# Kernel tuning notes

Measured on AMD Instinct MI355X. Metric: run time of the kernel, lower is better.

The kernel has to match this reference:

```python
import jax, jax.numpy as jnp
import numpy as np

N = 100000
D = 128
R = 4
E = 1600000
LN_EPS = 1e-3  # keras LayerNormalization default epsilon


def setup_inputs() -> dict:
    key = jax.random.key(0)
    ks = jax.random.split(key, 12)
    return {
        "node_embeddings": jax.random.normal(ks[0], (N, D), jnp.float32),
        "rel_embeddings": jax.random.normal(ks[1], (R, D), jnp.float32),
        "adj_rows": jax.random.randint(ks[2], (R, E), 0, N, jnp.int32),
        "adj_cols": jax.random.randint(ks[3], (R, E), 0, N, jnp.int32),
        "adj_vals": jax.random.uniform(ks[4], (R, E), jnp.float32),
        "W_fuse": jax.random.normal(ks[5], (2 * D, D), jnp.float32) * 0.05,
        "b_fuse": jnp.zeros((D,), jnp.float32),
        "W_rel": jax.random.normal(ks[6], (R, D, D), jnp.float32) * 0.05,
        "b_rel": jnp.zeros((R, D), jnp.float32),
        "rel_weights": jnp.ones((R,), jnp.float32),
        "W_gate": jax.random.normal(ks[7], (D, D), jnp.float32) * 0.05,
        "b_gate": jnp.zeros((D,), jnp.float32),
        "ln_gamma": jnp.ones((D,), jnp.float32),
        "ln_beta": jnp.zeros((D,), jnp.float32),
    }


def reference(node_embeddings, rel_embeddings, adj_rows, adj_cols, adj_vals,
              W_fuse, b_fuse, W_rel, b_rel, rel_weights, W_gate, b_gate,
              ln_gamma, ln_beta):
    n = node_embeddings.shape[0]
    rel_outs = []
    for r in range(R):  # small fixed relation count, structurally distinct kernels
        # sparse-dense matmul: messages[i] = sum_j A_r[i,j] * X[j]
        gathered = adj_vals[r][:, None] * node_embeddings[adj_cols[r]]  # [E, D]
        messages = jax.ops.segment_sum(gathered, adj_rows[r], num_segments=n)  # [N, D]
        rel_vec = jnp.broadcast_to(rel_embeddings[r], messages.shape)
        cat = jnp.concatenate([messages, rel_vec], axis=-1)  # [N, 2D]
        fused = jax.nn.relu(cat @ W_fuse + b_fuse)  # [N, D]
        rel_outs.append(fused @ W_rel[r] + b_rel[r])  # relation-specific kernel
    stacked = jnp.stack(rel_outs, axis=0)  # [R, N, D]
    w = jax.nn.softmax(rel_weights)
    combined = jnp.einsum('r,rnd->nd', w, stacked)
    gate = jax.nn.sigmoid(node_embeddings @ W_gate + b_gate)
    x = node_embeddings + gate * combined
    mu = jnp.mean(x, axis=-1, keepdims=True)
    var = jnp.mean((x - mu) ** 2, axis=-1, keepdims=True)
    out = (x - mu) * jax.lax.rsqrt(var + LN_EPS) * ln_gamma + ln_beta
    return out  # dropout is identity at inference (training=None)
```

## Files before the change

### kernel.cpp

```cpp
#include <hip/hip_runtime.h>
#include <math.h>

#define N_NODES 100000
#define DIM 128
#define NREL 4
#define NEDGE 1600000
#define LN_EPS 1e-3f

#define NBUCK 196
#define BCAP 10240
#define P1_VPT 16
#define P1_EDGES 4096

typedef __attribute__((ext_vector_type(8))) short bf16x8;
typedef __attribute__((ext_vector_type(4))) float f32x4;

__device__ __forceinline__ float bf2f(unsigned short b) {
    return __uint_as_float(((unsigned int)b) << 16);
}
__device__ __forceinline__ unsigned short f2bf(float f) {
    unsigned int u = __float_as_uint(f);
    u += 0x7FFFu + ((u >> 16) & 1u);
    return (unsigned short)(u >> 16);
}

__global__ __launch_bounds__(512) void prep_kernel(
    const float* __restrict__ rel_emb, const float* __restrict__ W_fuse,
    const float* __restrict__ b_fuse, const float* __restrict__ rel_weights,
    float* __restrict__ bfr, float* __restrict__ wsm)
{
    int t = threadIdx.x;
    int r = t >> 7;
    int d = t & 127;
    float acc = b_fuse[d];
    for (int k = 0; k < DIM; ++k)
        acc += rel_emb[r * DIM + k] * W_fuse[(DIM + k) * DIM + d];
    bfr[r * DIM + d] = acc;
    if (t < NREL) {
        float m = rel_weights[0];
        for (int i = 1; i < NREL; ++i) m = fmaxf(m, rel_weights[i]);
        float s = 0.f;
        for (int i = 0; i < NREL; ++i) s += expf(rel_weights[i] - m);
        wsm[t] = expf(rel_weights[t] - m) / s;
    }
}

__global__ __launch_bounds__(256) void pack_kernel(
    const float* __restrict__ Wf, const float* __restrict__ Wr,
    const float* __restrict__ Wg,
    unsigned short* __restrict__ PH, unsigned short* __restrict__ PL)
{
    int mat = blockIdx.y;
    int idx = blockIdx.x * 256 + threadIdx.x;
    int j = idx & 7;
    int lane = (idx >> 3) & 63;
    int ntile = (idx >> 9) & 7;
    int kblk = idx >> 12;
    int k = kblk * 32 + (lane >> 4) * 8 + j;
    int n = ntile * 16 + (lane & 15);
    const float* src = (mat == 0) ? Wf :
                       (mat == 5) ? Wg : (Wr + (size_t)(mat - 1) * DIM * DIM);
    float w = src[k * DIM + n];
    unsigned short hi = f2bf(w);
    float lo = w - bf2f(hi);
    PH[mat * 16384 + idx] = hi;
    PL[mat * 16384 + idx] = f2bf(lo);
}

__global__ __launch_bounds__(256) void xb_kernel(
    const float* __restrict__ X, unsigned short* __restrict__ Xb)
{
    int idx = blockIdx.x * 256 + threadIdx.x;
    float4 f = ((const float4*)X)[idx];
    ushort4 o;
    o.x = f2bf(f.x); o.y = f2bf(f.y); o.z = f2bf(f.z); o.w = f2bf(f.w);
    ((ushort4*)Xb)[idx] = o;
}

__global__ __launch_bounds__(256) void binA_kernel(
    const int* __restrict__ arows, const int* __restrict__ acols,
    const float* __restrict__ avals,
    int* __restrict__ bcnt,
    unsigned long long* __restrict__ edges2)
{
    __shared__ int hist[256];
    __shared__ int hoff[256];
    __shared__ int gbase[NBUCK];
    __shared__ unsigned long long stage[P1_EDGES];
    __shared__ unsigned short sbid[P1_EDGES];

    int t = threadIdx.x;
    int rl = blockIdx.y;
    int e0 = blockIdx.x * P1_EDGES;

    hist[t] = 0;
    __syncthreads();

    int b[P1_VPT], rank[P1_VPT], rloc[P1_VPT];
    unsigned int pay[P1_VPT];
#pragma unroll
    for (int i = 0; i < P1_VPT; ++i) {
        int e = e0 + i * 256 + t;
        b[i] = -1;
        if (e < NEDGE) {
            size_t off = (size_t)rl * NEDGE + e;
            int row = arows[off];
            unsigned int vb = __float_as_uint(avals[off]);
            vb += 0x7FFFu + ((vb >> 16) & 1u);
            pay[i] = ((unsigned int)acols[off] << 15) | ((vb >> 16) & 0x7FFFu);
            b[i] = row >> 9;
            rloc[i] = row & 511;
            rank[i] = atomicAdd(&hist[b[i]], 1);
        }
    }
    __syncthreads();

    int v = hist[t];
    int run = v;
    hoff[t] = run;
    __syncthreads();
    for (int o = 1; o < 256; o <<= 1) {
        int other = (t >= o) ? hoff[t - o] : 0;
        __syncthreads();
        run += other;
        hoff[t] = run;
        __syncthreads();
    }
    hoff[t] = run - v;
    if (t < NBUCK) {
        int g = (v > 0) ? atomicAdd(&bcnt[rl * NBUCK + t], v) : 0;
        gbase[t] = (rl * NBUCK + t) * BCAP + g;
    }
    __syncthreads();

#pragma unroll
    for (int i = 0; i < P1_VPT; ++i) {
        if (b[i] >= 0) {
            int slot = hoff[b[i]] + rank[i];
            stage[slot] = ((unsigned long long)rloc[i] << 32) | pay[i];
            sbid[slot] = (unsigned short)b[i];
        }
    }
    __syncthreads();

    int total = hoff[NBUCK - 1] + hist[NBUCK - 1];
    for (int idx = t; idx < total; idx += 256) {
        int bb = sbid[idx];
        int gaddr = gbase[bb] + (idx - hoff[bb]);
        if (gaddr - (rl * NBUCK + bb) * BCAP < BCAP)
            edges2[gaddr] = stage[idx];
    }
}

__global__ __launch_bounds__(1024) void bscan_kernel(
    const int* __restrict__ bcnt, int* __restrict__ bstart)
{
    __shared__ int s[1024];
    int t = threadIdx.x;
    int v = (t < NREL * NBUCK) ? min(bcnt[t], BCAP) : 0;
    int run = v;
    s[t] = run;
    __syncthreads();
    for (int o = 1; o < 1024; o <<= 1) {
        int other = (t >= o) ? s[t - o] : 0;
        __syncthreads();
        run += other;
        s[t] = run;
        __syncthreads();
    }
    if (t < NREL * NBUCK) bstart[t] = run - v;
}

__global__ __launch_bounds__(256) void binB_kernel(
    const unsigned long long* __restrict__ edges2,
    const int* __restrict__ bcnt, const int* __restrict__ bstart,
    int* __restrict__ rowstart, unsigned int* __restrict__ edges)
{
    __shared__ int rcnt[512];
    __shared__ int rpos[512];
    __shared__ int sc[256];

    int t = threadIdx.x;
    int b = blockIdx.x, rl = blockIdx.y;
    int gb = rl * NBUCK + b;
    int cnt = min(bcnt[gb], BCAP);
    const unsigned long long* src = edges2 + (size_t)gb * BCAP;
    int row0 = b << 9;
    int nrows = min(512, N_NODES - row0);

    rcnt[t] = 0; rcnt[t + 256] = 0;
    __syncthreads();
    for (int e = t; e < cnt; e += 256)
        atomicAdd(&rcnt[(int)(src[e] >> 32)], 1);
    __syncthreads();

    int v0 = rcnt[2 * t], v1 = rcnt[2 * t + 1];
    int tsum = v0 + v1;
    int run = tsum;
    sc[t] = run;
    __syncthreads();
    for (int o = 1; o < 256; o <<= 1) {
        int other = (t >= o) ? sc[t - o] : 0;
        __syncthreads();
        run += other;
        sc[t] = run;
        __syncthreads();
    }
    int base = bstart[gb];
    int excl = base + run - tsum;
    rpos[2 * t] = excl;
    rpos[2 * t + 1] = excl + v0;
    __syncthreads();

    for (int i = t; i < nrows; i += 256)
        rowstart[rl * N_NODES + row0 + i] = rpos[i];
    __syncthreads();

    for (int e = t; e < cnt; e += 256) {
        unsigned long long s = src[e];
        int p = atomicAdd(&rpos[(int)(s >> 32)], 1);
        edges[p] = (unsigned int)s;
    }
}

#define FMA8(acc, v, q)                                    \
    acc[0] += v * __uint_as_float((q).x << 16);            \
    acc[1] += v * __uint_as_float((q).x & 0xFFFF0000u);    \
    acc[2] += v * __uint_as_float((q).y << 16);            \
    acc[3] += v * __uint_as_float((q).y & 0xFFFF0000u);    \
    acc[4] += v * __uint_as_float((q).z << 16);            \
    acc[5] += v * __uint_as_float((q).z & 0xFFFF0000u);    \
    acc[6] += v * __uint_as_float((q).w << 16);            \
    acc[7] += v * __uint_as_float((q).w & 0xFFFF0000u);

__global__ __launch_bounds__(256) void gather_kernel(
    const unsigned short* __restrict__ Xb,
    const int* __restrict__ rowstart,
    const unsigned int* __restrict__ edges,
    unsigned short* __restrict__ msgs)
{
    int t = threadIdx.x;
    int grp = t >> 4, lane = t & 15;
    int row = blockIdx.x * 16 + grp;
    int rl = blockIdx.y;
    int g = rl * N_NODES + row;
    int s = rowstart[g];
    int e = (g == NREL * N_NODES - 1) ? (NREL * NEDGE) : rowstart[g + 1];

    float a0[8], a1[8], a2[8], a3[8];
#pragma unroll
    for (int i = 0; i < 8; ++i) { a0[i] = 0.f; a1[i] = 0.f; a2[i] = 0.f; a3[i] = 0.f; }

    const uint4* Xb4 = (const uint4*)Xb;
    int ee = s;
    int nrem = e - s;
    if (nrem >= 4) {
        unsigned int p0 = edges[ee], p1 = edges[ee + 1],
                     p2 = edges[ee + 2], p3 = edges[ee + 3];
        while (nrem >= 4) {
            uint4 q0 = Xb4[((size_t)(p0 >> 15) << 4) + lane];
            uint4 q1 = Xb4[((size_t)(p1 >> 15) << 4) + lane];
            uint4 q2 = Xb4[((size_t)(p2 >> 15) << 4) + lane];
            uint4 q3 = Xb4[((size_t)(p3 >> 15) << 4) + lane];
            float v0 = __uint_as_float((p0 & 0x7FFFu) << 16);
            float v1 = __uint_as_float((p1 & 0x7FFFu) << 16);
            float v2 = __uint_as_float((p2 & 0x7FFFu) << 16);
            float v3 = __uint_as_float((p3 & 0x7FFFu) << 16);
            nrem -= 4; ee += 4;
            if (nrem >= 4) {
                p0 = edges[ee]; p1 = edges[ee + 1];
                p2 = edges[ee + 2]; p3 = edges[ee + 3];
            }
            FMA8(a0, v0, q0)
            FMA8(a1, v1, q1)
            FMA8(a2, v2, q2)
            FMA8(a3, v3, q3)
        }
    }
    while (nrem > 0) {
        unsigned int p = edges[ee];
        uint4 q = Xb4[((size_t)(p >> 15) << 4) + lane];
        float v = __uint_as_float((p & 0x7FFFu) << 16);
        FMA8(a0, v, q)
        ++ee; --nrem;
    }
#pragma unroll
    for (int i = 0; i < 8; ++i) a0[i] += a1[i] + a2[i] + a3[i];
    uint4 o;
    o.x = ((unsigned int)f2bf(a0[1]) << 16) | f2bf(a0[0]);
    o.y = ((unsigned int)f2bf(a0[3]) << 16) | f2bf(a0[2]);
    o.z = ((unsigned int)f2bf(a0[5]) << 16) | f2bf(a0[4]);
    o.w = ((unsigned int)f2bf(a0[7]) << 16) | f2bf(a0[6]);
    ((uint4*)(msgs + ((size_t)g << 7)))[lane] = o;
}

__global__ __launch_bounds__(256) void gemm_mfma_kernel(
    const unsigned short* __restrict__ msgs,
    const unsigned short* __restrict__ Xb,
    const float* __restrict__ X,
    const unsigned short* __restrict__ PH,
    const unsigned short* __restrict__ PL,
    const float* __restrict__ bfr,
    const float* __restrict__ br,
    const float* __restrict__ wsm,
    const float* __restrict__ bg,
    const float* __restrict__ gamma,
    const float* __restrict__ beta,
    float* __restrict__ out)
{
    __shared__ unsigned short sA[32 * 128];
    __shared__ unsigned short sBh[32 * 128];
    __shared__ unsigned short sBl[32 * 128];
    __shared__ float sX[32 * 132];
    __shared__ float red[32][8], red2[32][8];
    __shared__ float smu[32], srs[32];

    int t = threadIdx.x;
    int row0 = blockIdx.x * 32;
    int wv = t >> 6;
    int l = t & 63;
    int lq = l >> 4;
    int lm = l & 15;

    f32x4 comb[2][2];
#pragma unroll
    for (int mt = 0; mt < 2; ++mt)
#pragma unroll
        for (int ni = 0; ni < 2; ++ni)
#pragma unroll
            for (int r = 0; r < 4; ++r) comb[mt][ni][r] = 0.f;

    for (int rl = 0; rl < NREL; ++rl) {
        __syncthreads();

        {
            const uint4* src = (const uint4*)msgs +
                ((size_t)(rl * N_NODES + row0) << 4);
#pragma unroll
            for (int it = 0; it < 2; ++it) {
                int i = t + it * 256;
                int row = i >> 4, ck = i & 15;
                uint4 v = src[i];
                *(uint4*)((char*)sA + row * 256 + ((ck * 16) ^ ((row & 7) << 4))) = v;
            }
        }
        __syncthreads();

        f32x4 acc[2][2];
#pragma unroll
        for (int mt = 0; mt < 2; ++mt)
#pragma unroll
            for (int ni = 0; ni < 2; ++ni)
#pragma unroll
                for (int r = 0; r < 4; ++r) acc[mt][ni][r] = 0.f;

#pragma unroll
        for (int kb = 0; kb < 4; ++kb) {
            int c0 = kb * 64 + lq * 16;
            int r0 = lm, r1 = 16 + lm;
            bf16x8 a0 = *(const bf16x8*)((char*)sA + r0 * 256 + (c0 ^ ((r0 & 7) << 4)));
            bf16x8 a1 = *(const bf16x8*)((char*)sA + r1 * 256 + (c0 ^ ((r1 & 7) << 4)));
#pragma unroll
            for (int ni = 0; ni < 2; ++ni) {
                int nt = wv * 2 + ni;
                int fi = ((kb * 8 + nt) * 64 + l) << 3;
                bf16x8 bh = *(const bf16x8*)(PH + fi);
                bf16x8 bl = *(const bf16x8*)(PL + fi);
                acc[0][ni] = __builtin_amdgcn_mfma_f32_16x16x32_bf16(a0, bh, acc[0][ni], 0, 0, 0);
                acc[1][ni] = __builtin_amdgcn_mfma_f32_16x16x32_bf16(a1, bh, acc[1][ni], 0, 0, 0);
                acc[0][ni] = __builtin_amdgcn_mfma_f32_16x16x32_bf16(a0, bl, acc[0][ni], 0, 0, 0);
                acc[1][ni] = __builtin_amdgcn_mfma_f32_16x16x32_bf16(a1, bl, acc[1][ni], 0, 0, 0);
            }
        }

#pragma unroll
        for (int mt = 0; mt < 2; ++mt)
#pragma unroll
        for (int ni = 0; ni < 2; ++ni) {
            int colg = (wv * 2 + ni) * 16 + lm;
            float b = bfr[rl * DIM + colg];
#pragma unroll
            for (int r = 0; r < 4; ++r) {
                int row = mt * 16 + lq * 4 + r;
                float v = fmaxf(acc[mt][ni][r] + b, 0.f);
                unsigned short hi = f2bf(v);
                unsigned short lo = f2bf(v - bf2f(hi));
                int off = row * 256 + ((colg * 2) ^ ((row & 7) << 4));
                *(unsigned short*)((char*)sBh + off) = hi;
                *(unsigned short*)((char*)sBl + off) = lo;
            }
        }
        __syncthreads();

        const unsigned short* ph2 = PH + (size_t)(1 + rl) * 16384;
        const unsigned short* pl2 = PL + (size_t)(1 + rl) * 16384;
#pragma unroll
        for (int mt = 0; mt < 2; ++mt)
#pragma unroll
            for (int ni = 0; ni < 2; ++ni)
#pragma unroll
                for (int r = 0; r < 4; ++r) acc[mt][ni][r] = 0.f;

#pragma unroll
        for (int kb = 0; kb < 4; ++kb) {
            int c0 = kb * 64 + lq * 16;
            int r0 = lm, r1 = 16 + lm;
            int o0 = r0 * 256 + (c0 ^ ((r0 & 7) << 4));
            int o1 = r1 * 256 + (c0 ^ ((r1 & 7) << 4));
            bf16x8 ah0 = *(const bf16x8*)((char*)sBh + o0);
            bf16x8 ah1 = *(const bf16x8*)((char*)sBh + o1);
            bf16x8 al0 = *(const bf16x8*)((char*)sBl + o0);
            bf16x8 al1 = *(const bf16x8*)((char*)sBl + o1);
#pragma unroll
            for (int ni = 0; ni < 2; ++ni) {
                int nt = wv * 2 + ni;
                int fi = ((kb * 8 + nt) * 64 + l) << 3;
                bf16x8 bh = *(const bf16x8*)(ph2 + fi);
                bf16x8 bl = *(const bf16x8*)(pl2 + fi);
                acc[0][ni] = __builtin_amdgcn_mfma_f32_16x16x32_bf16(ah0, bh, acc[0][ni], 0, 0, 0);
                acc[1][ni] = __builtin_amdgcn_mfma_f32_16x16x32_bf16(ah1, bh, acc[1][ni], 0, 0, 0);
                acc[0][ni] = __builtin_amdgcn_mfma_f32_16x16x32_bf16(ah0, bl, acc[0][ni], 0, 0, 0);
                acc[1][ni] = __builtin_amdgcn_mfma_f32_16x16x32_bf16(ah1, bl, acc[1][ni], 0, 0, 0);
                acc[0][ni] = __builtin_amdgcn_mfma_f32_16x16x32_bf16(al0, bh, acc[0][ni], 0, 0, 0);
                acc[1][ni] = __builtin_amdgcn_mfma_f32_16x16x32_bf16(al1, bh, acc[1][ni], 0, 0, 0);
            }
        }
        {
            float wr_ = wsm[rl];
#pragma unroll
            for (int mt = 0; mt < 2; ++mt)
#pragma unroll
            for (int ni = 0; ni < 2; ++ni) {
                int colg = (wv * 2 + ni) * 16 + lm;
                float b = br[rl * DIM + colg];
#pragma unroll
                for (int r = 0; r < 4; ++r)
                    comb[mt][ni][r] += wr_ * (acc[mt][ni][r] + b);
            }
        }
    }

    __syncthreads();
    {
        const uint4* src = (const uint4*)Xb + ((size_t)row0 << 4);
#pragma unroll
        for (int it = 0; it < 2; ++it) {
            int i = t + it * 256;
            int row = i >> 4, ck = i & 15;
            uint4 v = src[i];
            *(uint4*)((char*)sA + row * 256 + ((ck * 16) ^ ((row & 7) << 4))) = v;
        }
    }
    __syncthreads();

    f32x4 accg[2][2];
#pragma unroll
    for (int mt = 0; mt < 2; ++mt)
#pragma unroll
        for (int ni = 0; ni < 2; ++ni)
#pragma unroll
            for (int r = 0; r < 4; ++r) accg[mt][ni][r] = 0.f;

    const unsigned short* phg = PH + (size_t)5 * 16384;
    const unsigned short* plg = PL + (size_t)5 * 16384;
#pragma unroll
    for (int kb = 0; kb < 4; ++kb) {
        int c0 = kb * 64 + lq * 16;
        int r0 = lm, r1 = 16 + lm;
        bf16x8 a0 = *(const bf16x8*)((char*)sA + r0 * 256 + (c0 ^ ((r0 & 7) << 4)));
        bf16x8 a1 = *(const bf16x8*)((char*)sA + r1 * 256 + (c0 ^ ((r1 & 7) << 4)));
#pragma unroll
        for (int ni = 0; ni < 2; ++ni) {
            int nt = wv * 2 + ni;
            int fi = ((kb * 8 + nt) * 64 + l) << 3;
            bf16x8 bh = *(const bf16x8*)(phg + fi);
            bf16x8 bl = *(const bf16x8*)(plg + fi);
            accg[0][ni] = __builtin_amdgcn_mfma_f32_16x16x32_bf16(a0, bh, accg[0][ni], 0, 0, 0);
            accg[1][ni] = __builtin_amdgcn_mfma_f32_16x16x32_bf16(a1, bh, accg[1][ni], 0, 0, 0);
            accg[0][ni] = __builtin_amdgcn_mfma_f32_16x16x32_bf16(a0, bl, accg[0][ni], 0, 0, 0);
            accg[1][ni] = __builtin_amdgcn_mfma_f32_16x16x32_bf16(a1, bl, accg[1][ni], 0, 0, 0);
        }
    }

#pragma unroll
    for (int mt = 0; mt < 2; ++mt)
#pragma unroll
    for (int ni = 0; ni < 2; ++ni) {
        int colg = (wv * 2 + ni) * 16 + lm;
        float bgv = bg[colg];
#pragma unroll
        for (int r = 0; r < 4; ++r) {
            int row = mt * 16 + lq * 4 + r;
            float g = 1.f / (1.f + expf(-(accg[mt][ni][r] + bgv)));
            float xv = X[(size_t)(row0 + row) * DIM + colg] + g * comb[mt][ni][r];
            sX[row * 132 + colg] = xv;
        }
    }
    __syncthreads();

    {
        int row = t >> 3, seg = t & 7;
        float s = 0.f, s2 = 0.f;
#pragma unroll
        for (int i = 0; i < 16; ++i) {
            float v = sX[row * 132 + seg * 16 + i];
            s += v; s2 += v * v;
        }
        red[row][seg] = s;
        red2[row][seg] = s2;
    }
    __syncthreads();
    if ((t & 7) == 0) {
        int row = t >> 3;
        float ts = 0.f, ts2 = 0.f;
#pragma unroll
        for (int i = 0; i < 8; ++i) { ts += red[row][i]; ts2 += red2[row][i]; }
        float mu = ts / DIM;
        float var = ts2 / DIM - mu * mu;
        smu[row] = mu;
        srs[row] = rsqrtf(var + LN_EPS);
    }
    __syncthreads();
    {
        float gm0 = gamma[l], gm1 = gamma[l + 64];
        float bt0 = beta[l],  bt1 = beta[l + 64];
#pragma unroll
        for (int rr = 0; rr < 8; ++rr) {
            int row = wv * 8 + rr;
            size_t gi = (size_t)(row0 + row) * DIM + l;
            out[gi]      = (sX[row * 132 + l]      - smu[row]) * srs[row] * gm0 + bt0;
            out[gi + 64] = (sX[row * 132 + l + 64] - smu[row]) * srs[row] * gm1 + bt1;
        }
    }
}

__global__ __launch_bounds__(256) void hist_kernel(
    const int* __restrict__ arows, int* __restrict__ counts)
{
    int e = blockIdx.x * 256 + threadIdx.x;
    int rl = blockIdx.y;
    if (e < NEDGE) {
        int row = arows[(size_t)rl * NEDGE + e];
        atomicAdd(&counts[rl * N_NODES + row], 1);
    }
}

__global__ __launch_bounds__(256) void scan1_kernel(
    int* __restrict__ counts, int* __restrict__ chunksums, int M)
{
    __shared__ int s[256];
    int chunk = blockIdx.x, t = threadIdx.x;
    int base = chunk * 1024 + t * 4;
    int v0 = (base + 0 < M) ? counts[base + 0] : 0;
    int v1 = (base + 1 < M) ? counts[base + 1] : 0;
    int v2 = (base + 2 < M) ? counts[base + 2] : 0;
    int v3 = (base + 3 < M) ? counts[base + 3] : 0;
    int p1 = v0, p2 = v0 + v1, p3 = v0 + v1 + v2, tsum = p3 + v3;
    int run = tsum;
    s[t] = run;
    __syncthreads();
    for (int off = 1; off < 256; off <<= 1) {
        int other = (t >= off) ? s[t - off] : 0;
        __syncthreads();
        run += other;
        s[t] = run;
        __syncthreads();
    }
    int excl = run - tsum;
    if (t == 255) chunksums[chunk] = run;
    if (base + 0 < M) counts[base + 0] = excl;
    if (base + 1 < M) counts[base + 1] = excl + p1;
    if (base + 2 < M) counts[base + 2] = excl + p2;
    if (base + 3 < M) counts[base + 3] = excl + p3;
}

__global__ __launch_bounds__(512) void scan2_kernel(
    int* __restrict__ chunksums, int nchunks)
{
    __shared__ int s[512];
    int t = threadIdx.x;
    int v = (t < nchunks) ? chunksums[t] : 0;
    int run = v;
    s[t] = run;
    __syncthreads();
    for (int off = 1; off < 512; off <<= 1) {
        int other = (t >= off) ? s[t - off] : 0;
        __syncthreads();
        run += other;
        s[t] = run;
        __syncthreads();
    }
    if (t < nchunks) chunksums[t] = run - v;
}

__global__ __launch_bounds__(256) void reorder_kernel(
    const int* __restrict__ arows, const int* __restrict__ acols,
    const float* __restrict__ avals,
    int* __restrict__ counts, const int* __restrict__ chunks,
    unsigned int* __restrict__ edges)
{
    int e = blockIdx.x * 256 + threadIdx.x;
    int rl = blockIdx.y;
    if (e < NEDGE) {
        size_t off = (size_t)rl * NEDGE + e;
        int row = arows[off];
        int g = rl * N_NODES + row;
        int pos = atomicAdd(&counts[g], 1) + chunks[g >> 10];
        unsigned int vb = __float_as_uint(avals[off]);
        vb += 0x7FFFu + ((vb >> 16) & 1u);
        edges[pos] = ((unsigned int)acols[off] << 15) | ((vb >> 16) & 0x7FFFu);
    }
}

__global__ __launch_bounds__(256) void mega_kernel(
    const unsigned short* __restrict__ Xb,
    const float* __restrict__ X,
    const int* __restrict__ counts,
    const int* __restrict__ chunks,
    const unsigned int* __restrict__ edges,
    const float* __restrict__ W1,
    const float* __restrict__ bfr,
    const float* __restrict__ Wr,
    const float* __restrict__ br,
    const float* __restrict__ wsm,
    const float* __restrict__ Wg,
    const float* __restrict__ bg,
    const float* __restrict__ gamma,
    const float* __restrict__ beta,
    float* __restrict__ out)
{
    __shared__ float sIn[32][DIM];
    __shared__ float red[32][8], red2[32][8];
    __shared__ float smu[32], srs[32];

    int t = threadIdx.x;
    int row0 = blockIdx.x * 32;
    int w = t >> 6;
    int l = t & 63;
    int grp = t >> 5, lane = t & 31;

    float comb_acc[8][2];
#pragma unroll
    for (int rr = 0; rr < 8; ++rr) { comb_acc[rr][0] = 0.f; comb_acc[rr][1] = 0.f; }

    for (int rl = 0; rl < NREL; ++rl) {
        __syncthreads();
#pragma unroll
        for (int i = 0; i < 4; ++i) {
            int ln = grp * 4 + i;
            int g = rl * N_NODES + row0 + ln;
            int s = (g == 0) ? 0 : counts[g - 1] + chunks[(g - 1) >> 10];
            int e = counts[g] + chunks[g >> 10];
            float4 a0 = make_float4(0.f, 0.f, 0.f, 0.f);
            int ee = s;
            for (; ee < e; ++ee) {
                unsigned int p0 = edges[ee];
                const ushort4* x0 = (const ushort4*)(Xb + ((size_t)(p0 >> 15) << 7));
                ushort4 q0 = x0[lane];
                float v0 = __uint_as_float((p0 & 0x7FFFu) << 16);
                a0.x += v0 * bf2f(q0.x); a0.y += v0 * bf2f(q0.y);
                a0.z += v0 * bf2f(q0.z); a0.w += v0 * bf2f(q0.w);
            }
            ((float4*)&sIn[ln][0])[lane] = a0;
        }
        __syncthreads();

        float acc1[8][2];
#pragma unroll
        for (int rr = 0; rr < 8; ++rr) { acc1[rr][0] = 0.f; acc1[rr][1] = 0.f; }
        for (int k4 = 0; k4 < DIM / 4; ++k4) {
            float wa[4], wb4[4];
#pragma unroll
            for (int j = 0; j < 4; ++j) {
                wa[j]  = W1[(k4 * 4 + j) * DIM + l];
                wb4[j] = W1[(k4 * 4 + j) * DIM + l + 64];
            }
#pragma unroll
            for (int rr = 0; rr < 8; ++rr) {
                float4 m = *(const float4*)&sIn[w * 8 + rr][k4 * 4];
                acc1[rr][0] += m.x * wa[0]  + m.y * wa[1]  + m.z * wa[2]  + m.w * wa[3];
                acc1[rr][1] += m.x * wb4[0] + m.y * wb4[1] + m.z * wb4[2] + m.w * wb4[3];
            }
        }
        __syncthreads();
        {
            float b0 = bfr[rl * DIM + l], b1 = bfr[rl * DIM + l + 64];
#pragma unroll
            for (int rr = 0; rr < 8; ++rr) {
                sIn[w * 8 + rr][l]      = fmaxf(acc1[rr][0] + b0, 0.f);
                sIn[w * 8 + rr][l + 64] = fmaxf(acc1[rr][1] + b1, 0.f);
            }
        }
        __syncthreads();

        const float* W2 = Wr + (size_t)rl * DIM * DIM;
        float acc2[8][2];
#pragma unroll
        for (int rr = 0; rr < 8; ++rr) { acc2[rr][0] = 0.f; acc2[rr][1] = 0.f; }
        for (int k4 = 0; k4 < DIM / 4; ++k4) {
            float wa[4], wb4[4];
#pragma unroll
            for (int j = 0; j < 4; ++j) {
                wa[j]  = W2[(k4 * 4 + j) * DIM + l];
                wb4[j] = W2[(k4 * 4 + j) * DIM + l + 64];
            }
#pragma unroll
            for (int rr = 0; rr < 8; ++rr) {
                float4 m = *(const float4*)&sIn[w * 8 + rr][k4 * 4];
                acc2[rr][0] += m.x * wa[0]  + m.y * wa[1]  + m.z * wa[2]  + m.w * wa[3];
                acc2[rr][1] += m.x * wb4[0] + m.y * wb4[1] + m.z * wb4[2] + m.w * wb4[3];
            }
        }
        {
            float wr_ = wsm[rl];
            float bb0 = br[rl * DIM + l], bb1 = br[rl * DIM + l + 64];
#pragma unroll
            for (int rr = 0; rr < 8; ++rr) {
                comb_acc[rr][0] += wr_ * (acc2[rr][0] + bb0);
                comb_acc[rr][1] += wr_ * (acc2[rr][1] + bb1);
            }
        }
    }

    __syncthreads();
    {
        const float4* src = (const float4*)(X + (size_t)row0 * DIM);
        float4* dst = (float4*)&sIn[0][0];
        for (int i = t; i < 32 * DIM / 4; i += 256) dst[i] = src[i];
    }
    __syncthreads();

    float accg[8][2];
#pragma unroll
    for (int rr = 0; rr < 8; ++rr) { accg[rr][0] = 0.f; accg[rr][1] = 0.f; }
    for (int k4 = 0; k4 < DIM / 4; ++k4) {
        float wa[4], wb4[4];
#pragma unroll
        for (int j = 0; j < 4; ++j) {
            wa[j]  = Wg[(k4 * 4 + j) * DIM + l];
            wb4[j] = Wg[(k4 * 4 + j) * DIM + l + 64];
        }
#pragma unroll
        for (int rr = 0; rr < 8; ++rr) {
            float4 m = *(const float4*)&sIn[w * 8 + rr][k4 * 4];
            accg[rr][0] += m.x * wa[0]  + m.y * wa[1]  + m.z * wa[2]  + m.w * wa[3];
            accg[rr][1] += m.x * wb4[0] + m.y * wb4[1] + m.z * wb4[2] + m.w * wb4[3];
        }
    }
    float xv[8][2];
    {
        float bg0 = bg[l], bg1 = bg[l + 64];
#pragma unroll
        for (int rr = 0; rr < 8; ++rr) {
            int row = w * 8 + rr;
            float g0 = 1.f / (1.f + expf(-(accg[rr][0] + bg0)));
            float g1 = 1.f / (1.f + expf(-(accg[rr][1] + bg1)));
            xv[rr][0] = sIn[row][l]      + g0 * comb_acc[rr][0];
            xv[rr][1] = sIn[row][l + 64] + g1 * comb_acc[rr][1];
        }
    }
    __syncthreads();
#pragma unroll
    for (int rr = 0; rr < 8; ++rr) {
        sIn[w * 8 + rr][l]      = xv[rr][0];
        sIn[w * 8 + rr][l + 64] = xv[rr][1];
    }
    __syncthreads();

    {
        int row = t >> 3, seg = t & 7;
        float s = 0.f, s2 = 0.f;
#pragma unroll
        for (int i = 0; i < 16; ++i) {
            float v = sIn[row][seg * 16 + i];
            s += v; s2 += v * v;
        }
        red[row][seg] = s;
        red2[row][seg] = s2;
    }
    __syncthreads();
    if ((t & 7) == 0) {
        int row = t >> 3;
        float ts = 0.f, ts2 = 0.f;
#pragma unroll
        for (int i = 0; i < 8; ++i) { ts += red[row][i]; ts2 += red2[row][i]; }
        float mu = ts / DIM;
        float var = ts2 / DIM - mu * mu;
        smu[row] = mu;
        srs[row] = rsqrtf(var + LN_EPS);
    }
    __syncthreads();
    {
        float gm0 = gamma[l], gm1 = gamma[l + 64];
        float bt0 = beta[l],  bt1 = beta[l + 64];
#pragma unroll
        for (int rr = 0; rr < 8; ++rr) {
            int row = w * 8 + rr;
            size_t gi = (size_t)(row0 + row) * DIM + l;
            out[gi]      = (sIn[row][l]      - smu[row]) * srs[row] * gm0 + bt0;
            out[gi + 64] = (sIn[row][l + 64] - smu[row]) * srs[row] * gm1 + bt1;
        }
    }
}

extern "C" void kernel_launch(void* const* d_in, const int* in_sizes, int n_in,
                              void* d_out, int out_size, void* d_ws, size_t ws_size,
                              hipStream_t stream) {
    const float* X     = (const float*)d_in[0];
    const float* rel   = (const float*)d_in[1];
    const int*   arows = (const int*)d_in[2];
    const int*   acols = (const int*)d_in[3];
    const float* avals = (const float*)d_in[4];
    const float* Wf    = (const float*)d_in[5];
    const float* bf    = (const float*)d_in[6];
    const float* Wr    = (const float*)d_in[7];
    const float* br    = (const float*)d_in[8];
    const float* rw    = (const float*)d_in[9];
    const float* Wg    = (const float*)d_in[10];
    const float* bg    = (const float*)d_in[11];
    const float* gamma = (const float*)d_in[12];
    const float* beta  = (const float*)d_in[13];
    float* out = (float*)d_out;

    const size_t XB_B = (size_t)N_NODES * DIM * 2;
    const size_t ED_B = (size_t)NREL * NEDGE * 4;
    const size_t CT_B = (size_t)NREL * N_NODES * 4;
    char* p = (char*)d_ws;
    unsigned short* Xb     = (unsigned short*)p;  p += XB_B;
    unsigned int*   edges  = (unsigned int*)p;    p += ED_B;
    int*            counts = (int*)p;             p += CT_B;
    int*            chunks = (int*)p;             p += 512 * 4;
    float*          bfr    = (float*)p;           p += NREL * DIM * 4;
    float*          wsm    = (float*)p;           p += 64 * 4;
    int*            bcnt   = (int*)p;             p += NREL * NBUCK * 4;
    int*            bstart = (int*)p;             p += (NREL * NBUCK + 1) * 4;
    unsigned short* PH     = (unsigned short*)p;  p += 6 * 16384 * 2;
    unsigned short* PL     = (unsigned short*)p;  p += 6 * 16384 * 2;
    size_t off = (size_t)(p - (char*)d_ws);
    off = (off + 255) & ~(size_t)255;
    unsigned short* msgs = (unsigned short*)((char*)d_ws + off);
    unsigned long long* edges2 = (unsigned long long*)msgs;
    const size_t need = off + (size_t)NREL * N_NODES * DIM * 2;
    const bool split = (ws_size >= need);

    prep_kernel<<<1, 512, 0, stream>>>(rel, Wf, bf, rw, bfr, wsm);
    pack_kernel<<<dim3(64, 6), 256, 0, stream>>>(Wf, Wr, Wg, PH, PL);
    xb_kernel<<<N_NODES * DIM / 4 / 256, 256, 0, stream>>>(X, Xb);

    if (split) {
        hipMemsetAsync(bcnt, 0, (size_t)NREL * NBUCK * sizeof(int), stream);
        const int AB = (NEDGE + P1_EDGES - 1) / P1_EDGES;
        binA_kernel<<<dim3(AB, NREL), 256, 0, stream>>>(
            arows, acols, avals, bcnt, edges2);
        bscan_kernel<<<1, 1024, 0, stream>>>(bcnt, bstart);
        binB_kernel<<<dim3(NBUCK, NREL), 256, 0, stream>>>(
            edges2, bcnt, bstart, counts, edges);
        gather_kernel<<<dim3(N_NODES / 16, NREL), 256, 0, stream>>>(
            Xb, counts, edges, msgs);
        gemm_mfma_kernel<<<N_NODES / 32, 256, 0, stream>>>(
            msgs, Xb, X, PH, PL, bfr, br, wsm, bg, gamma, beta, out);
    } else {
        const int EB = (NEDGE + 255) / 256;
        const int M = NREL * N_NODES;
        const int nch = (M + 1023) / 1024;
        hipMemsetAsync(counts, 0, (size_t)M * sizeof(int), stream);
        hist_kernel<<<dim3(EB, NREL), 256, 0, stream>>>(arows, counts);
        scan1_kernel<<<nch, 256, 0, stream>>>(counts, chunks, M);
        scan2_kernel<<<1, 512, 0, stream>>>(chunks, nch);
        reorder_kernel<<<dim3(EB, NREL), 256, 0, stream>>>(
            arows, acols, avals, counts, chunks, edges);
        mega_kernel<<<N_NODES / 32, 256, 0, stream>>>(
            Xb, X, counts, chunks, edges, Wf, bfr, Wr, br, wsm,
            Wg, bg, gamma, beta, out);
    }
}
```

Measured before the change: 659.0 us.

## Precompute X·W_fuse before gather so SpMM aggregates projected features

Uses linearity, A·X·W = A·(X·W), to compute Y = X·W_fuse[:D] once per node in a new y_kernel before the sparse aggregation. The gather then sums rows of Y, adds the relation bias and applies ReLU, so the per-relation fuse GEMM leaves the final GEMM kernel. That kernel now runs one GEMM per relation and prefetches the next relation's messages into registers. Edge loads and message stores become nontemporal. The trade-off is extra bf16 rounding, since Y is stored in bf16 before aggregation, and the gate GEMM now converts X to bf16 inside the kernel.

```diff
diff --git a/kernel.cpp b/kernel.cpp
--- a/kernel.cpp
+++ b/kernel.cpp
@@ -14,6 +14,7 @@
 
 typedef __attribute__((ext_vector_type(8))) short bf16x8;
 typedef __attribute__((ext_vector_type(4))) float f32x4;
+typedef __attribute__((ext_vector_type(4))) unsigned int u32x4;
 
 __device__ __forceinline__ float bf2f(unsigned short b) {
     return __uint_as_float(((unsigned int)b) << 16);
@@ -77,6 +78,99 @@
     ((ushort4*)Xb)[idx] = o;
 }
 
+__global__ __launch_bounds__(256) void y_kernel(
+    const float* __restrict__ X,
+    const unsigned short* __restrict__ PH,
+    const unsigned short* __restrict__ PL,
+    unsigned short* __restrict__ Yb)
+{
+    __shared__ unsigned short sXh[32 * 128];
+    __shared__ unsigned short sXl[32 * 128];
+
+    int t = threadIdx.x;
+    int row0 = blockIdx.x * 32;
+    int wv = t >> 6, l = t & 63, lq = l >> 4, lm = l & 15;
+
+    const float4* Xs = (const float4*)(X + (size_t)row0 * DIM);
+#pragma unroll
+    for (int it = 0; it < 2; ++it) {
+        int i = t + it * 256;
+        float4 f0 = Xs[2 * i];
+        float4 f1 = Xs[2 * i + 1];
+        float e[8] = {f0.x, f0.y, f0.z, f0.w, f1.x, f1.y, f1.z, f1.w};
+        unsigned short h[8], lo[8];
+#pragma unroll
+        for (int j = 0; j < 8; ++j) {
+            h[j] = f2bf(e[j]);
+            lo[j] = f2bf(e[j] - bf2f(h[j]));
+        }
+        uint4 hv, lv;
+        hv.x = ((unsigned int)h[1] << 16) | h[0];
+        hv.y = ((unsigned int)h[3] << 16) | h[2];
+        hv.z = ((unsigned int)h[5] << 16) | h[4];
+        hv.w = ((unsigned int)h[7] << 16) | h[6];
+        lv.x = ((unsigned int)lo[1] << 16) | lo[0];
+        lv.y = ((unsigned int)lo[3] << 16) | lo[2];
+        lv.z = ((unsigned int)lo[5] << 16) | lo[4];
+        lv.w = ((unsigned int)lo[7] << 16) | lo[6];
+        int row = i >> 4, ck = i & 15;
+        int off = row * 256 + ((ck * 16) ^ ((row & 7) << 4));
+        *(uint4*)((char*)sXh + off) = hv;
+        *(uint4*)((char*)sXl + off) = lv;
+    }
+    __syncthreads();
+
+    f32x4 acc[2][2];
+#pragma unroll
+    for (int mt = 0; mt < 2; ++mt)
+#pragma unroll
+        for (int ni = 0; ni < 2; ++ni)
+#pragma unroll
+            for (int r = 0; r < 4; ++r) acc[mt][ni][r] = 0.f;
+
+#pragma unroll
+    for (int kb = 0; kb < 4; ++kb) {
+        int c0 = kb * 64 + lq * 16;
+        int r0 = lm, r1 = 16 + lm;
+        int o0 = r0 * 256 + (c0 ^ ((r0 & 7) << 4));
+        int o1 = r1 * 256 + (c0 ^ ((r1 & 7) << 4));
+        bf16x8 ah0 = *(const bf16x8*)((char*)sXh + o0);
+        bf16x8 ah1 = *(const bf16x8*)((char*)sXh + o1);
+        bf16x8 al0 = *(const bf16x8*)((char*)sXl + o0);
+        bf16x8 al1 = *(const bf16x8*)((char*)sXl + o1);
+#pragma unroll
+        for (int ni = 0; ni < 2; ++ni) {
+            int nt_ = wv * 2 + ni;
+            int fi = ((kb * 8 + nt_) * 64 + l) << 3;
+            bf16x8 bh = *(const bf16x8*)(PH + fi);
+            bf16x8 bl = *(const bf16x8*)(PL + fi);
+            acc[0][ni] = __builtin_amdgcn_mfma_f32_16x16x32_bf16(ah0, bh, acc[0][ni], 0, 0, 0);
+            acc[1][ni] = __builtin_amdgcn_mfma_f32_16x16x32_bf16(ah1, bh, acc[1][ni], 0, 0, 0);
+            acc[0][ni] = __builtin_amdgcn_mfma_f32_16x16x32_bf16(ah0, bl, acc[0][ni], 0, 0, 0);
+            acc[1][ni] = __builtin_amdgcn_mfma_f32_16x16x32_bf16(ah1, bl, acc[1][ni], 0, 0, 0);
+            acc[0][ni] = __builtin_amdgcn_mfma_f32_16x16x32_bf16(al0, bh, acc[0][ni], 0, 0, 0);
+            acc[1][ni] = __builtin_amdgcn_mfma_f32_16x16x32_bf16(al1, bh, acc[1][ni], 0, 0, 0);
+        }
+    }
+    __syncthreads();
+#pragma unroll
+    for (int mt = 0; mt < 2; ++mt)
+#pragma unroll
+    for (int ni = 0; ni < 2; ++ni) {
+        int colg = (wv * 2 + ni) * 16 + lm;
+#pragma unroll
+        for (int r = 0; r < 4; ++r) {
+            int row = mt * 16 + lq * 4 + r;
+            sXh[row * 128 + colg] = f2bf(acc[mt][ni][r]);
+        }
+    }
+    __syncthreads();
+    uint4* dst = (uint4*)(Yb + (size_t)row0 * DIM);
+    const uint4* s4 = (const uint4*)sXh;
+    dst[t] = s4[t];
+    dst[t + 256] = s4[t + 256];
+}
+
 __global__ __launch_bounds__(256) void binA_kernel(
     const int* __restrict__ arows, const int* __restrict__ acols,
     const float* __restrict__ avals,
@@ -234,9 +328,10 @@
     acc[7] += v * __uint_as_float((q).w & 0xFFFF0000u);
 
 __global__ __launch_bounds__(256) void gather_kernel(
-    const unsigned short* __restrict__ Xb,
+    const unsigned short* __restrict__ Yb,
     const int* __restrict__ rowstart,
     const unsigned int* __restrict__ edges,
+    const float* __restrict__ bfr,
     unsigned short* __restrict__ msgs)
 {
     int t = threadIdx.x;
@@ -251,25 +346,29 @@
 #pragma unroll
     for (int i = 0; i < 8; ++i) { a0[i] = 0.f; a1[i] = 0.f; a2[i] = 0.f; a3[i] = 0.f; }
 
-    const uint4* Xb4 = (const uint4*)Xb;
+    const uint4* Yb4 = (const uint4*)Yb;
     int ee = s;
     int nrem = e - s;
     if (nrem >= 4) {
-        unsigned int p0 = edges[ee], p1 = edges[ee + 1],
-                     p2 = edges[ee + 2], p3 = edges[ee + 3];
+        unsigned int p0 = __builtin_nontemporal_load(edges + ee);
+        unsigned int p1 = __builtin_nontemporal_load(edges + ee + 1);
+        unsigned int p2 = __builtin_nontemporal_load(edges + ee + 2);
+        unsigned int p3 = __builtin_nontemporal_load(edges + ee + 3);
         while (nrem >= 4) {
-            uint4 q0 = Xb4[((size_t)(p0 >> 15) << 4) + lane];
-            uint4 q1 = Xb4[((size_t)(p1 >> 15) << 4) + lane];
-            uint4 q2 = Xb4[((size_t)(p2 >> 15) << 4) + lane];
-            uint4 q3 = Xb4[((size_t)(p3 >> 15) << 4) + lane];
+            uint4 q0 = Yb4[((size_t)(p0 >> 15) << 4) + lane];
+            uint4 q1 = Yb4[((size_t)(p1 >> 15) << 4) + lane];
+            uint4 q2 = Yb4[((size_t)(p2 >> 15) << 4) + lane];
+            uint4 q3 = Yb4[((size_t)(p3 >> 15) << 4) + lane];
             float v0 = __uint_as_float((p0 & 0x7FFFu) << 16);
             float v1 = __uint_as_float((p1 & 0x7FFFu) << 16);
             float v2 = __uint_as_float((p2 & 0x7FFFu) << 16);
             float v3 = __uint_as_float((p3 & 0x7FFFu) << 16);
             nrem -= 4; ee += 4;
             if (nrem >= 4) {
-                p0 = edges[ee]; p1 = edges[ee + 1];
-                p2 = edges[ee + 2]; p3 = edges[ee + 3];
+                p0 = __builtin_nontemporal_load(edges + ee);
+                p1 = __builtin_nontemporal_load(edges + ee + 1);
+                p2 = __builtin_nontemporal_load(edges + ee + 2);
+                p3 = __builtin_nontemporal_load(edges + ee + 3);
             }
             FMA8(a0, v0, q0)
             FMA8(a1, v1, q1)
@@ -278,29 +377,34 @@
         }
     }
     while (nrem > 0) {
-        unsigned int p = edges[ee];
-        uint4 q = Xb4[((size_t)(p >> 15) << 4) + lane];
+        unsigned int p = __builtin_nontemporal_load(edges + ee);
+        uint4 q = Yb4[((size_t)(p >> 15) << 4) + lane];
         float v = __uint_as_float((p & 0x7FFFu) << 16);
         FMA8(a0, v, q)
         ++ee; --nrem;
     }
 #pragma unroll
     for (int i = 0; i < 8; ++i) a0[i] += a1[i] + a2[i] + a3[i];
-    uint4 o;
-    o.x = ((unsigned int)f2bf(a0[1]) << 16) | f2bf(a0[0]);
-    o.y = ((unsigned int)f2bf(a0[3]) << 16) | f2bf(a0[2]);
-    o.z = ((unsigned int)f2bf(a0[5]) << 16) | f2bf(a0[4]);
-    o.w = ((unsigned int)f2bf(a0[7]) << 16) | f2bf(a0[6]);
-    ((uint4*)(msgs + ((size_t)g << 7)))[lane] = o;
-}
-
-__global__ __launch_bounds__(256) void gemm_mfma_kernel(
+
+    const float4* bb = (const float4*)(bfr + rl * DIM + lane * 8);
+    float4 b0 = bb[0], b1 = bb[1];
+    float f0 = fmaxf(a0[0] + b0.x, 0.f), f1 = fmaxf(a0[1] + b0.y, 0.f);
+    float f2 = fmaxf(a0[2] + b0.z, 0.f), f3 = fmaxf(a0[3] + b0.w, 0.f);
+    float f4 = fmaxf(a0[4] + b1.x, 0.f), f5 = fmaxf(a0[5] + b1.y, 0.f);
+    float f6 = fmaxf(a0[6] + b1.z, 0.f), f7 = fmaxf(a0[7] + b1.w, 0.f);
+    u32x4 o;
+    o[0] = ((unsigned int)f2bf(f1) << 16) | f2bf(f0);
+    o[1] = ((unsigned int)f2bf(f3) << 16) | f2bf(f2);
+    o[2] = ((unsigned int)f2bf(f5) << 16) | f2bf(f4);
+    o[3] = ((unsigned int)f2bf(f7) << 16) | f2bf(f6);
+    __builtin_nontemporal_store(o, (u32x4*)(msgs + ((size_t)g << 7)) + lane);
+}
+
+__global__ __launch_bounds__(256) void gemm2_kernel(
     const unsigned short* __restrict__ msgs,
-    const unsigned short* __restrict__ Xb,
     const float* __restrict__ X,
     const unsigned short* __restrict__ PH,
     const unsigned short* __restrict__ PL,
-    const float* __restrict__ bfr,
     const float* __restrict__ br,
     const float* __restrict__ wsm,
     const float* __restrict__ bg,
@@ -308,19 +412,14 @@
     const float* __restrict__ beta,
     float* __restrict__ out)
 {
-    __shared__ unsigned short sA[32 * 128];
-    __shared__ unsigned short sBh[32 * 128];
-    __shared__ unsigned short sBl[32 * 128];
     __shared__ float sX[32 * 132];
     __shared__ float red[32][8], red2[32][8];
     __shared__ float smu[32], srs[32];
+    unsigned short* sB = (unsigned short*)sX;
 
     int t = threadIdx.x;
     int row0 = blockIdx.x * 32;
-    int wv = t >> 6;
-    int l = t & 63;
-    int lq = l >> 4;
-    int lm = l & 15;
+    int wv = t >> 6, l = t & 63, lq = l >> 4, lm = l & 15;
 
     f32x4 comb[2][2];
 #pragma unroll
@@ -330,70 +429,36 @@
 #pragma unroll
             for (int r = 0; r < 4; ++r) comb[mt][ni][r] = 0.f;
 
+    uint4 m0, m1;
+    {
+        const uint4* src = (const uint4*)msgs + ((size_t)row0 << 4);
+        m0 = src[t]; m1 = src[t + 256];
+    }
+    float4 xa, xb_, xc, xd;
+
     for (int rl = 0; rl < NREL; ++rl) {
         __syncthreads();
-
         {
+            int i0 = t, i1 = t + 256;
+            int row = i0 >> 4, ck = i0 & 15;
+            *(uint4*)((char*)sB + row * 256 + ((ck * 16) ^ ((row & 7) << 4))) = m0;
+            row = i1 >> 4; ck = i1 & 15;
+            *(uint4*)((char*)sB + row * 256 + ((ck * 16) ^ ((row & 7) << 4))) = m1;
+        }
+        if (rl < NREL - 1) {
             const uint4* src = (const uint4*)msgs +
-                ((size_t)(rl * N_NODES + row0) << 4);
-#pragma unroll
-            for (int it = 0; it < 2; ++it) {
-                int i = t + it * 256;
-                int row = i >> 4, ck = i & 15;
-                uint4 v = src[i];
-                *(uint4*)((char*)sA + row * 256 + ((ck * 16) ^ ((row & 7) << 4))) = v;
-            }
-        }
-        __syncthreads();
-
-        f32x4 acc[2][2];
-#pragma unroll
-        for (int mt = 0; mt < 2; ++mt)
-#pragma unroll
-            for (int ni = 0; ni < 2; ++ni)
-#pragma unroll
-                for (int r = 0; r < 4; ++r) acc[mt][ni][r] = 0.f;
-
-#pragma unroll
-        for (int kb = 0; kb < 4; ++kb) {
-            int c0 = kb * 64 + lq * 16;
-            int r0 = lm, r1 = 16 + lm;
-            bf16x8 a0 = *(const bf16x8*)((char*)sA + r0 * 256 + (c0 ^ ((r0 & 7) << 4)));
-            bf16x8 a1 = *(const bf16x8*)((char*)sA + r1 * 256 + (c0 ^ ((r1 & 7) << 4)));
-#pragma unroll
-            for (int ni = 0; ni < 2; ++ni) {
-                int nt = wv * 2 + ni;
-                int fi = ((kb * 8 + nt) * 64 + l) << 3;
-                bf16x8 bh = *(const bf16x8*)(PH + fi);
-                bf16x8 bl = *(const bf16x8*)(PL + fi);
-                acc[0][ni] = __builtin_amdgcn_mfma_f32_16x16x32_bf16(a0, bh, acc[0][ni], 0, 0, 0);
-                acc[1][ni] = __builtin_amdgcn_mfma_f32_16x16x32_bf16(a1, bh, acc[1][ni], 0, 0, 0);
-                acc[0][ni] = __builtin_amdgcn_mfma_f32_16x16x32_bf16(a0, bl, acc[0][ni], 0, 0, 0);
-                acc[1][ni] = __builtin_amdgcn_mfma_f32_16x16x32_bf16(a1, bl, acc[1][ni], 0, 0, 0);
-            }
-        }
-
-#pragma unroll
-        for (int mt = 0; mt < 2; ++mt)
-#pragma unroll
-        for (int ni = 0; ni < 2; ++ni) {
-            int colg = (wv * 2 + ni) * 16 + lm;
-            float b = bfr[rl * DIM + colg];
-#pragma unroll
-            for (int r = 0; r < 4; ++r) {
-                int row = mt * 16 + lq * 4 + r;
-                float v = fmaxf(acc[mt][ni][r] + b, 0.f);
-                unsigned short hi = f2bf(v);
-                unsigned short lo = f2bf(v - bf2f(hi));
-                int off = row * 256 + ((colg * 2) ^ ((row & 7) << 4));
-                *(unsigned short*)((char*)sBh + off) = hi;
-                *(unsigned short*)((char*)sBl + off) = lo;
-            }
+                ((size_t)((rl + 1) * N_NODES + row0) << 4);
+            m0 = src[t]; m1 = src[t + 256];
+        } else {
+            const float4* Xs = (const float4*)(X + (size_t)row0 * DIM);
+            xa = Xs[2 * t];       xb_ = Xs[2 * t + 1];
+            xc = Xs[2 * (t + 256)]; xd = Xs[2 * (t + 256) + 1];
         }
         __syncthreads();
 
         const unsigned short* ph2 = PH + (size_t)(1 + rl) * 16384;
         const unsigned short* pl2 = PL + (size_t)(1 + rl) * 16384;
+        f32x4 acc[2][2];
 #pragma unroll
         for (int mt = 0; mt < 2; ++mt)
 #pragma unroll
@@ -407,22 +472,18 @@
             int r0 = lm, r1 = 16 + lm;
             int o0 = r0 * 256 + (c0 ^ ((r0 & 7) << 4));
             int o1 = r1 * 256 + (c0 ^ ((r1 & 7) << 4));
-            bf16x8 ah0 = *(const bf16x8*)((char*)sBh + o0);
-            bf16x8 ah1 = *(const bf16x8*)((char*)sBh + o1);
-            bf16x8 al0 = *(const bf16x8*)((char*)sBl + o0);
-            bf16x8 al1 = *(const bf16x8*)((char*)sBl + o1);
+            bf16x8 a0v = *(const bf16x8*)((char*)sB + o0);
+            bf16x8 a1v = *(const bf16x8*)((char*)sB + o1);
 #pragma unroll
             for (int ni = 0; ni < 2; ++ni) {
-                int nt = wv * 2 + ni;
-                int fi = ((kb * 8 + nt) * 64 + l) << 3;
+                int nt_ = wv * 2 + ni;
+                int fi = ((kb * 8 + nt_) * 64 + l) << 3;
                 bf16x8 bh = *(const bf16x8*)(ph2 + fi);
                 bf16x8 bl = *(const bf16x8*)(pl2 + fi);
-                acc[0][ni] = __builtin_amdgcn_mfma_f32_16x16x32_bf16(ah0, bh, acc[0][ni], 0, 0, 0);
-                acc[1][ni] = __builtin_amdgcn_mfma_f32_16x16x32_bf16(ah1, bh, acc[1][ni], 0, 0, 0);
-                acc[0][ni] = __builtin_amdgcn_mfma_f32_16x16x32_bf16(ah0, bl, acc[0][ni], 0, 0, 0);
-                acc[1][ni] = __builtin_amdgcn_mfma_f32_16x16x32_bf16(ah1, bl, acc[1][ni], 0, 0, 0);
-                acc[0][ni] = __builtin_amdgcn_mfma_f32_16x16x32_bf16(al0, bh, acc[0][ni], 0, 0, 0);
-                acc[1][ni] = __builtin_amdgcn_mfma_f32_16x16x32_bf16(al1, bh, acc[1][ni], 0, 0, 0);
+                acc[0][ni] = __builtin_amdgcn_mfma_f32_16x16x32_bf16(a0v, bh, acc[0][ni], 0, 0, 0);
+                acc[1][ni] = __builtin_amdgcn_mfma_f32_16x16x32_bf16(a1v, bh, acc[1][ni], 0, 0, 0);
+                acc[0][ni] = __builtin_amdgcn_mfma_f32_16x16x32_bf16(a0v, bl, acc[0][ni], 0, 0, 0);
+                acc[1][ni] = __builtin_amdgcn_mfma_f32_16x16x32_bf16(a1v, bl, acc[1][ni], 0, 0, 0);
             }
         }
         {
@@ -442,14 +503,21 @@
 
     __syncthreads();
     {
-        const uint4* src = (const uint4*)Xb + ((size_t)row0 << 4);
-#pragma unroll
-        for (int it = 0; it < 2; ++it) {
-            int i = t + it * 256;
-            int row = i >> 4, ck = i & 15;
-            uint4 v = src[i];
-            *(uint4*)((char*)sA + row * 256 + ((ck * 16) ^ ((row & 7) << 4))) = v;
-        }
+        float e0[8] = {xa.x, xa.y, xa.z, xa.w, xb_.x, xb_.y, xb_.z, xb_.w};
+        uint4 hv;
+        hv.x = ((unsigned int)f2bf(e0[1]) << 16) | f2bf(e0[0]);
+        hv.y = ((unsigned int)f2bf(e0[3]) << 16) | f2bf(e0[2]);
+        hv.z = ((unsigned int)f2bf(e0[5]) << 16) | f2bf(e0[4]);
+        hv.w = ((unsigned int)f2bf(e0[7]) << 16) | f2bf(e0[6]);
+        int i = t, row = i >> 4, ck = i & 15;
+        *(uint4*)((char*)sB + row * 256 + ((ck * 16) ^ ((row & 7) << 4))) = hv;
+        float e1[8] = {xc.x, xc.y, xc.z, xc.w, xd.x, xd.y, xd.z, xd.w};
+        hv.x = ((unsigned int)f2bf(e1[1]) << 16) | f2bf(e1[0]);
+        hv.y = ((unsigned int)f2bf(e1[3]) << 16) | f2bf(e1[2]);
+        hv.z = ((unsigned int)f2bf(e1[5]) << 16) | f2bf(e1[4]);
+        hv.w = ((unsigned int)f2bf(e1[7]) << 16) | f2bf(e1[6]);
+        i = t + 256; row = i >> 4; ck = i & 15;
+        *(uint4*)((char*)sB + row * 256 + ((ck * 16) ^ ((row & 7) << 4))) = hv;
     }
     __syncthreads();
 
@@ -467,20 +535,21 @@
     for (int kb = 0; kb < 4; ++kb) {
         int c0 = kb * 64 + lq * 16;
         int r0 = lm, r1 = 16 + lm;
-        bf16x8 a0 = *(const bf16x8*)((char*)sA + r0 * 256 + (c0 ^ ((r0 & 7) << 4)));
-        bf16x8 a1 = *(const bf16x8*)((char*)sA + r1 * 256 + (c0 ^ ((r1 & 7) << 4)));
+        bf16x8 a0v = *(const bf16x8*)((char*)sB + r0 * 256 + (c0 ^ ((r0 & 7) << 4)));
+        bf16x8 a1v = *(const bf16x8*)((char*)sB + r1 * 256 + (c0 ^ ((r1 & 7) << 4)));
 #pragma unroll
         for (int ni = 0; ni < 2; ++ni) {
-            int nt = wv * 2 + ni;
-            int fi = ((kb * 8 + nt) * 64 + l) << 3;
+            int nt_ = wv * 2 + ni;
+            int fi = ((kb * 8 + nt_) * 64 + l) << 3;
             bf16x8 bh = *(const bf16x8*)(phg + fi);
             bf16x8 bl = *(const bf16x8*)(plg + fi);
-            accg[0][ni] = __builtin_amdgcn_mfma_f32_16x16x32_bf16(a0, bh, accg[0][ni], 0, 0, 0);
-            accg[1][ni] = __builtin_amdgcn_mfma_f32_16x16x32_bf16(a1, bh, accg[1][ni], 0, 0, 0);
-            accg[0][ni] = __builtin_amdgcn_mfma_f32_16x16x32_bf16(a0, bl, accg[0][ni], 0, 0, 0);
-            accg[1][ni] = __builtin_amdgcn_mfma_f32_16x16x32_bf16(a1, bl, accg[1][ni], 0, 0, 0);
-        }
-    }
+            accg[0][ni] = __builtin_amdgcn_mfma_f32_16x16x32_bf16(a0v, bh, accg[0][ni], 0, 0, 0);
+            accg[1][ni] = __builtin_amdgcn_mfma_f32_16x16x32_bf16(a1v, bh, accg[1][ni], 0, 0, 0);
+            accg[0][ni] = __builtin_amdgcn_mfma_f32_16x16x32_bf16(a0v, bl, accg[0][ni], 0, 0, 0);
+            accg[1][ni] = __builtin_amdgcn_mfma_f32_16x16x32_bf16(a1v, bl, accg[1][ni], 0, 0, 0);
+        }
+    }
+    __syncthreads();
 
 #pragma unroll
     for (int mt = 0; mt < 2; ++mt)
@@ -826,7 +895,7 @@
     const size_t ED_B = (size_t)NREL * NEDGE * 4;
     const size_t CT_B = (size_t)NREL * N_NODES * 4;
     char* p = (char*)d_ws;
-    unsigned short* Xb     = (unsigned short*)p;  p += XB_B;
+    unsigned short* Yb     = (unsigned short*)p;  p += XB_B;
     unsigned int*   edges  = (unsigned int*)p;    p += ED_B;
     int*            counts = (int*)p;             p += CT_B;
     int*            chunks = (int*)p;             p += 512 * 4;
@@ -845,9 +914,9 @@
 
     prep_kernel<<<1, 512, 0, stream>>>(rel, Wf, bf, rw, bfr, wsm);
     pack_kernel<<<dim3(64, 6), 256, 0, stream>>>(Wf, Wr, Wg, PH, PL);
-    xb_kernel<<<N_NODES * DIM / 4 / 256, 256, 0, stream>>>(X, Xb);
 
     if (split) {
+        y_kernel<<<N_NODES / 32, 256, 0, stream>>>(X, PH, PL, Yb);
         hipMemsetAsync(bcnt, 0, (size_t)NREL * NBUCK * sizeof(int), stream);
         const int AB = (NEDGE + P1_EDGES - 1) / P1_EDGES;
         binA_kernel<<<dim3(AB, NREL), 256, 0, stream>>>(
@@ -856,10 +925,11 @@
         binB_kernel<<<dim3(NBUCK, NREL), 256, 0, stream>>>(
             edges2, bcnt, bstart, counts, edges);
         gather_kernel<<<dim3(N_NODES / 16, NREL), 256, 0, stream>>>(
-            Xb, counts, edges, msgs);
-        gemm_mfma_kernel<<<N_NODES / 32, 256, 0, stream>>>(
-            msgs, Xb, X, PH, PL, bfr, br, wsm, bg, gamma, beta, out);
+            Yb, counts, edges, bfr, msgs);
+        gemm2_kernel<<<N_NODES / 32, 256, 0, stream>>>(
+            msgs, X, PH, PL, br, wsm, bg, gamma, beta, out);
     } else {
+        xb_kernel<<<N_NODES * DIM / 4 / 256, 256, 0, stream>>>(X, Yb);
         const int EB = (NEDGE + 255) / 256;
         const int M = NREL * N_NODES;
         const int nch = (M + 1023) / 1024;
@@ -870,7 +940,7 @@
         reorder_kernel<<<dim3(EB, NREL), 256, 0, stream>>>(
             arows, acols, avals, counts, chunks, edges);
         mega_kernel<<<N_NODES / 32, 256, 0, stream>>>(
-            Xb, X, counts, chunks, edges, Wf, bfr, Wr, br, wsm,
+            Yb, X, counts, chunks, edges, Wf, bfr, Wr, br, wsm,
             Wg, bg, gamma, beta, out);
     }
 }
```

Measured after the change: 637.0 us. -3.3%, faster.
